# Performance work log

Measured on AMD Instinct MI355X. Metric: run time of the kernel, lower is better.

The kernel has to match this reference:

```python
import jax, jax.numpy as jnp
import numpy as np

NUM_CLASSES = 81
POS_THR = 0.5
NEG_THR = 0.1
TOTAL = 512        # roi_training_total_num_samples
MAX_POS = 128      # roi_training_max_pos_samples
SIGMA = 1.0
CLS_W = 1.0
REG_W = 1.0
BBOX_MEAN = jnp.array([0.0, 0.0, 0.0, 0.0], dtype=jnp.float32)
BBOX_STD = jnp.array([0.1, 0.1, 0.2, 0.2], dtype=jnp.float32)
N_PROP = 65536
N_GT = 64
IMG = 1024.0


def _make_boxes(key, n):
    k1, k2, k3, k4 = jax.random.split(key, 4)
    cx = jax.random.uniform(k1, (n,), minval=150.0, maxval=870.0)
    cy = jax.random.uniform(k2, (n,), minval=150.0, maxval=870.0)
    w = jax.random.uniform(k3, (n,), minval=40.0, maxval=200.0)
    h = jax.random.uniform(k4, (n,), minval=40.0, maxval=200.0)
    return jnp.stack([cx - w / 2, cy - h / 2, cx + w / 2, cy + h / 2], axis=1)


def _sanitize(b):
    b = jnp.clip(b, 0.0, IMG)
    x1, y1, x2, y2 = b[:, 0], b[:, 1], b[:, 2], b[:, 3]
    return jnp.stack([x1, y1, jnp.maximum(x2, x1 + 1.0), jnp.maximum(y2, y1 + 1.0)], axis=1)


def setup_inputs() -> dict:
    key = jax.random.key(0)
    ks = jax.random.split(key, 8)
    gt_bboxes = _make_boxes(ks[0], N_GT)
    gt_labels = jax.random.randint(ks[1], (N_GT,), 1, NUM_CLASSES).astype(jnp.int32)
    # proposals: 4096 light-jittered gt copies (positives), 16384 medium jitter
    # (iou in [0.1,0.5) band), rest random -> realistic pos/neg mix
    n_pos, n_med = 4096, 16384
    base_pos = gt_bboxes[jnp.arange(n_pos) % N_GT]
    base_med = gt_bboxes[jnp.arange(n_med) % N_GT]
    p_pos = base_pos + jax.random.uniform(ks[2], (n_pos, 4), minval=-15.0, maxval=15.0)
    p_med = base_med + jax.random.uniform(ks[3], (n_med, 4), minval=-80.0, maxval=80.0)
    p_rand = _make_boxes(ks[4], N_PROP - n_pos - n_med)
    rpn_proposals_bboxes = _sanitize(jnp.concatenate([p_pos, p_med, p_rand], axis=0))
    roi_score = jax.random.normal(ks[5], (N_PROP, NUM_CLASSES), dtype=jnp.float32)
    roi_bboxes_txtytwth = jax.random.normal(ks[6], (N_PROP, NUM_CLASSES, 4), dtype=jnp.float32)
    image_shape = jnp.array([IMG, IMG], dtype=jnp.float32)
    return {
        "image_shape": image_shape,
        "rpn_proposals_bboxes": rpn_proposals_bboxes,
        "roi_score": roi_score,
        "roi_bboxes_txtytwth": roi_bboxes_txtytwth,
        "gt_bboxes": gt_bboxes,
        "gt_labels": gt_labels,
    }


def pairwise_iou(a, b):
    # a: [N,4], b: [G,4] in (x1,y1,x2,y2)
    area_a = (a[:, 2] - a[:, 0]) * (a[:, 3] - a[:, 1])
    area_b = (b[:, 2] - b[:, 0]) * (b[:, 3] - b[:, 1])
    lt = jnp.maximum(a[:, None, :2], b[None, :, :2])
    rb = jnp.minimum(a[:, None, 2:], b[None, :, 2:])
    wh = jnp.clip(rb - lt, 0.0)
    inter = wh[..., 0] * wh[..., 1]
    return inter / (area_a[:, None] + area_b[None, :] - inter + 1e-8)


def encode_bbox(props, gts):
    pw = props[:, 2] - props[:, 0]
    ph = props[:, 3] - props[:, 1]
    pcx = props[:, 0] + 0.5 * pw
    pcy = props[:, 1] + 0.5 * ph
    gw = gts[:, 2] - gts[:, 0]
    gh = gts[:, 3] - gts[:, 1]
    gcx = gts[:, 0] + 0.5 * gw
    gcy = gts[:, 1] + 0.5 * gh
    t = jnp.stack([(gcx - pcx) / pw, (gcy - pcy) / ph,
                   jnp.log(gw / pw), jnp.log(gh / ph)], axis=1)
    return (t - BBOX_MEAN) / BBOX_STD


def smooth_l1(diff, sigma):
    s2 = sigma * sigma
    ad = jnp.abs(diff)
    return jnp.where(ad < 1.0 / s2, 0.5 * s2 * diff * diff, ad - 0.5 / s2)


def sample_rois(proposals, gt_bboxes):
    # IoU-threshold sampler with deterministic (index-order) selection and
    # static output size TOTAL. Returns (idx[TOTAL], labels[TOTAL], gt_idx[TOTAL], num_pos)
    n = proposals.shape[0]
    iou = pairwise_iou(proposals, gt_bboxes)          # [N,G]
    max_iou = iou.max(axis=1)
    gt_idx = jnp.argmax(iou, axis=1)
    pos_mask = max_iou >= POS_THR
    neg_mask = (max_iou < POS_THR) & (max_iou >= NEG_THR)
    num_pos = jnp.minimum(pos_mask.sum(), MAX_POS)
    ar = jnp.arange(n)
    pos_order = jnp.argsort(jnp.where(pos_mask, ar, ar + n))
    neg_order = jnp.argsort(jnp.where(neg_mask, ar, ar + n))
    slot = jnp.arange(TOTAL)
    is_pos = slot < num_pos
    idx = jnp.where(is_pos, pos_order[jnp.clip(slot, 0, n - 1)],
                    neg_order[jnp.clip(slot - num_pos, 0, n - 1)])
    labels = is_pos.astype(jnp.int32)
    return idx, labels, gt_idx[idx], is_pos


def reference(image_shape, rpn_proposals_bboxes, roi_score, roi_bboxes_txtytwth,
              gt_bboxes, gt_labels):
    idx, labels, gt_sel, is_pos = sample_rois(rpn_proposals_bboxes, gt_bboxes)
    # classification loss over all TOTAL samples (negatives get label 0)
    logits = roi_score[idx]                              # [T,C]
    cls_labels = gt_labels[gt_sel] * labels              # [T]
    logp = jax.nn.log_softmax(logits, axis=-1)
    ce = -jnp.take_along_axis(logp, cls_labels[:, None], axis=1)[:, 0]
    cls_loss = CLS_W * ce.mean()
    pred = roi_bboxes_txtytwth[idx, gt_sel]              # [T,4]
    targets = encode_bbox(jax.lax.stop_gradient(rpn_proposals_bboxes[idx]),
                          jax.lax.stop_gradient(gt_bboxes[gt_sel]))
    sl1 = smooth_l1(pred - targets, SIGMA)               # [T,4]
    m = is_pos.astype(pred.dtype)[:, None]
    reg_loss = REG_W * jnp.sum(sl1 * m) / float(TOTAL)
    return (cls_loss, reg_loss)
```

## Files before the change

kernel.cpp:

```cpp
#include <hip/hip_runtime.h>
#include <cstdint>

#define N_PROP 65536
#define N_GT 64
#define NUM_CLASSES 81
#define TOTAL_SLOTS 512
#define MAX_POS 128

__global__ __launch_bounds__(256) void iou_cat_kernel(
    const float* __restrict__ props,
    const float* __restrict__ gts,
    int* __restrict__ code_ws) {
  __shared__ float4 sgt[N_GT];
  __shared__ float sarea[N_GT];
  int tid = threadIdx.x;
  if (tid < N_GT) {
    float4 g = ((const float4*)gts)[tid];
    sgt[tid] = g;
    sarea[tid] = (g.z - g.x) * (g.w - g.y);
  }
  __syncthreads();
  int i = blockIdx.x * blockDim.x + tid;
  if (i >= N_PROP) return;
  float4 p = ((const float4*)props)[i];
  float area_a = (p.z - p.x) * (p.w - p.y);
  float best = -1.0f;
  int bg = 0;
  for (int g = 0; g < N_GT; ++g) {
    float4 q = sgt[g];
    float ltx = fmaxf(p.x, q.x);
    float lty = fmaxf(p.y, q.y);
    float rbx = fminf(p.z, q.z);
    float rby = fminf(p.w, q.w);
    float wx = fmaxf(rbx - ltx, 0.0f);
    float wy = fmaxf(rby - lty, 0.0f);
    float inter = wx * wy;
    float denom = area_a + sarea[g] - inter + 1e-8f;
    float iou = inter / denom;
    if (iou > best) { best = iou; bg = g; }
  }
  int cat = (best >= 0.5f) ? 2 : ((best >= 0.1f) ? 1 : 0);
  code_ws[i] = (cat << 8) | bg;
}

__global__ __launch_bounds__(1024) void select_loss_kernel(
    const float* __restrict__ props,
    const float* __restrict__ scores,
    const float* __restrict__ deltas,
    const float* __restrict__ gts,
    const int* __restrict__ gt_labels,
    const int* __restrict__ code_ws,
    float* __restrict__ out) {
  __shared__ int pos_list[MAX_POS];
  __shared__ int neg_list[TOTAL_SLOTS];
  __shared__ int nn_list[TOTAL_SLOTS];
  __shared__ int wsum_p[16], wsum_n[16], wsum_nn[16];
  __shared__ int base_p, base_n, base_nn;
  __shared__ float red[1024];
  __shared__ float ce_sum_sh;

  int tid = threadIdx.x;
  if (tid == 0) { base_p = 0; base_n = 0; base_nn = 0; }
  __syncthreads();

  int lane = tid & 63;
  int wave = tid >> 6;
  uint64_t lmask = (1ULL << lane) - 1ULL;

  for (int c = 0; c < N_PROP / 1024; ++c) {
    if (base_p >= MAX_POS && base_n >= TOTAL_SLOTS && base_nn >= TOTAL_SLOTS)
      break;
    int i = c * 1024 + tid;
    int code = code_ws[i];
    int cat = code >> 8;
    bool isp = (cat == 2);
    bool isn = (cat == 1);
    bool isnn = !isn;
    uint64_t bp = __ballot(isp);
    uint64_t bn = __ballot(isn);
    uint64_t bnn = __ballot(isnn);
    if (lane == 0) {
      wsum_p[wave] = __popcll(bp);
      wsum_n[wave] = __popcll(bn);
      wsum_nn[wave] = __popcll(bnn);
    }
    __syncthreads();
    int wp = 0, wn = 0, wnn = 0;
    for (int w = 0; w < wave; ++w) {
      wp += wsum_p[w];
      wn += wsum_n[w];
      wnn += wsum_nn[w];
    }
    if (isp) {
      int r = base_p + wp + __popcll(bp & lmask);
      if (r < MAX_POS) pos_list[r] = i;
    }
    if (isn) {
      int r = base_n + wn + __popcll(bn & lmask);
      if (r < TOTAL_SLOTS) neg_list[r] = i;
    }
    if (isnn) {
      int r = base_nn + wnn + __popcll(bnn & lmask);
      if (r < TOTAL_SLOTS) nn_list[r] = i;
    }
    __syncthreads();
    if (tid == 0) {
      int tp = 0, tn = 0, tnn = 0;
      for (int w = 0; w < 16; ++w) {
        tp += wsum_p[w];
        tn += wsum_n[w];
        tnn += wsum_nn[w];
      }
      base_p += tp;
      base_n += tn;
      base_nn += tnn;
    }
    __syncthreads();
  }

  int num_pos = min(base_p, MAX_POS);
  int neg_total = base_n;

  float ce = 0.0f, reg = 0.0f;
  if (tid < TOTAL_SLOTS) {
    int s = tid;
    bool is_pos = (s < num_pos);
    int i;
    if (is_pos) {
      i = pos_list[s];
    } else {
      int j = s - num_pos;
      i = (j < neg_total) ? neg_list[j] : nn_list[j - neg_total];
    }
    int g = code_ws[i] & 0xFF;

    int cls = is_pos ? gt_labels[g] : 0;
    const float* row = scores + (size_t)i * NUM_CLASSES;
    float m = -INFINITY;
    for (int k = 0; k < NUM_CLASSES; ++k) m = fmaxf(m, row[k]);
    float sum = 0.0f;
    for (int k = 0; k < NUM_CLASSES; ++k) sum += expf(row[k] - m);
    ce = -(row[cls] - m - logf(sum));

    const float* pr = props + 4 * i;
    float pw = pr[2] - pr[0];
    float ph = pr[3] - pr[1];
    float pcx = pr[0] + 0.5f * pw;
    float pcy = pr[1] + 0.5f * ph;
    const float* gb = gts + 4 * g;
    float gw = gb[2] - gb[0];
    float gh = gb[3] - gb[1];
    float gcx = gb[0] + 0.5f * gw;
    float gcy = gb[1] + 0.5f * gh;
    float t0 = ((gcx - pcx) / pw) / 0.1f;
    float t1 = ((gcy - pcy) / ph) / 0.1f;
    float t2 = logf(gw / pw) / 0.2f;
    float t3 = logf(gh / ph) / 0.2f;
    const float* dd = deltas + ((size_t)i * NUM_CLASSES + (size_t)g) * 4;
    float d0 = dd[0] - t0;
    float d1 = dd[1] - t1;
    float d2 = dd[2] - t2;
    float d3 = dd[3] - t3;
    float sl = 0.0f;
    float a;
    a = fabsf(d0); sl += (a < 1.0f) ? 0.5f * d0 * d0 : a - 0.5f;
    a = fabsf(d1); sl += (a < 1.0f) ? 0.5f * d1 * d1 : a - 0.5f;
    a = fabsf(d2); sl += (a < 1.0f) ? 0.5f * d2 * d2 : a - 0.5f;
    a = fabsf(d3); sl += (a < 1.0f) ? 0.5f * d3 * d3 : a - 0.5f;
    if (is_pos) reg = sl;
  }

  red[tid] = ce;
  __syncthreads();
  for (int off = 512; off >= 1; off >>= 1) {
    if (tid < off) red[tid] += red[tid + off];
    __syncthreads();
  }
  if (tid == 0) ce_sum_sh = red[0];
  __syncthreads();

  red[tid] = reg;
  __syncthreads();
  for (int off = 512; off >= 1; off >>= 1) {
    if (tid < off) red[tid] += red[tid + off];
    __syncthreads();
  }
  if (tid == 0) {
    out[0] = ce_sum_sh / (float)TOTAL_SLOTS;
    out[1] = red[0] / (float)TOTAL_SLOTS;
  }
}

extern "C" void kernel_launch(void* const* d_in, const int* in_sizes, int n_in,
                              void* d_out, int out_size, void* d_ws, size_t ws_size,
                              hipStream_t stream) {
  (void)in_sizes; (void)n_in; (void)out_size; (void)ws_size;
  const float* props = (const float*)d_in[1];
  const float* scores = (const float*)d_in[2];
  const float* deltas = (const float*)d_in[3];
  const float* gts = (const float*)d_in[4];
  const int* gt_labels = (const int*)d_in[5];
  float* out = (float*)d_out;
  int* code_ws = (int*)d_ws;

  iou_cat_kernel<<<N_PROP / 256, 256, 0, stream>>>(props, gts, code_ws);
  select_loss_kernel<<<1, 1024, 0, stream>>>(props, scores, deltas, gts,
                                             gt_labels, code_ws, out);
}
```

Before: 182.5 us.

## Split selection and loss into separate kernels with per-sample wavefront loss

Moves the per-sample cross-entropy and regression loss out of the single-block selection kernel into a new kernel with one 64-thread block per selected sample. Each block loads its score row in parallel, reduces max and sum-exp with wave shuffles, and accumulates both losses into the output with atomics. The selection kernel writes packed indices to workspace and zeroes the output. This removes the serial 81-element loops and the long block reductions on one workgroup, at the cost of an extra launch, atomic ordering nondeterminism, and __expf approximation.

```diff
diff --git a/kernel.cpp b/kernel.cpp
--- a/kernel.cpp
+++ b/kernel.cpp
@@ -21,7 +21,6 @@
   }
   __syncthreads();
   int i = blockIdx.x * blockDim.x + tid;
-  if (i >= N_PROP) return;
   float4 p = ((const float4*)props)[i];
   float area_a = (p.z - p.x) * (p.w - p.y);
   float best = -1.0f;
@@ -43,21 +42,15 @@
   code_ws[i] = (cat << 8) | bg;
 }
 
-__global__ __launch_bounds__(1024) void select_loss_kernel(
-    const float* __restrict__ props,
-    const float* __restrict__ scores,
-    const float* __restrict__ deltas,
-    const float* __restrict__ gts,
-    const int* __restrict__ gt_labels,
+__global__ __launch_bounds__(1024) void select_kernel(
     const int* __restrict__ code_ws,
+    int* __restrict__ sel_ws,
     float* __restrict__ out) {
   __shared__ int pos_list[MAX_POS];
   __shared__ int neg_list[TOTAL_SLOTS];
   __shared__ int nn_list[TOTAL_SLOTS];
   __shared__ int wsum_p[16], wsum_n[16], wsum_nn[16];
   __shared__ int base_p, base_n, base_nn;
-  __shared__ float red[1024];
-  __shared__ float ce_sum_sh;
 
   int tid = threadIdx.x;
   if (tid == 0) { base_p = 0; base_n = 0; base_nn = 0; }
@@ -121,7 +114,6 @@
   int num_pos = min(base_p, MAX_POS);
   int neg_total = base_n;
 
-  float ce = 0.0f, reg = 0.0f;
   if (tid < TOTAL_SLOTS) {
     int s = tid;
     bool is_pos = (s < num_pos);
@@ -133,61 +125,74 @@
       i = (j < neg_total) ? neg_list[j] : nn_list[j - neg_total];
     }
     int g = code_ws[i] & 0xFF;
-
+    sel_ws[s] = i | (g << 17) | ((is_pos ? 1 : 0) << 23);
+  }
+  if (tid < 2) out[tid] = 0.0f;
+}
+
+__global__ __launch_bounds__(64) void loss_kernel(
+    const float* __restrict__ props,
+    const float* __restrict__ scores,
+    const float* __restrict__ deltas,
+    const float* __restrict__ gts,
+    const int* __restrict__ gt_labels,
+    const int* __restrict__ sel_ws,
+    float* __restrict__ out) {
+  int s = blockIdx.x;
+  int packed = sel_ws[s];
+  int i = packed & 0x1FFFF;
+  int g = (packed >> 17) & 0x3F;
+  bool is_pos = (packed >> 23) & 1;
+
+  int lane = threadIdx.x;
+  const float* row = scores + (size_t)i * NUM_CLASSES;
+  float v1 = row[lane];
+  bool has2 = (lane + 64) < NUM_CLASSES;
+  float v2 = has2 ? row[lane + 64] : -INFINITY;
+
+  float m = fmaxf(v1, v2);
+  #pragma unroll
+  for (int off = 32; off >= 1; off >>= 1)
+    m = fmaxf(m, __shfl_xor(m, off));
+
+  float e = __expf(v1 - m) + (has2 ? __expf(v2 - m) : 0.0f);
+  #pragma unroll
+  for (int off = 32; off >= 1; off >>= 1)
+    e += __shfl_xor(e, off);
+
+  if (lane == 0) {
     int cls = is_pos ? gt_labels[g] : 0;
-    const float* row = scores + (size_t)i * NUM_CLASSES;
-    float m = -INFINITY;
-    for (int k = 0; k < NUM_CLASSES; ++k) m = fmaxf(m, row[k]);
-    float sum = 0.0f;
-    for (int k = 0; k < NUM_CLASSES; ++k) sum += expf(row[k] - m);
-    ce = -(row[cls] - m - logf(sum));
-
-    const float* pr = props + 4 * i;
-    float pw = pr[2] - pr[0];
-    float ph = pr[3] - pr[1];
-    float pcx = pr[0] + 0.5f * pw;
-    float pcy = pr[1] + 0.5f * ph;
-    const float* gb = gts + 4 * g;
-    float gw = gb[2] - gb[0];
-    float gh = gb[3] - gb[1];
-    float gcx = gb[0] + 0.5f * gw;
-    float gcy = gb[1] + 0.5f * gh;
-    float t0 = ((gcx - pcx) / pw) / 0.1f;
-    float t1 = ((gcy - pcy) / ph) / 0.1f;
-    float t2 = logf(gw / pw) / 0.2f;
-    float t3 = logf(gh / ph) / 0.2f;
-    const float* dd = deltas + ((size_t)i * NUM_CLASSES + (size_t)g) * 4;
-    float d0 = dd[0] - t0;
-    float d1 = dd[1] - t1;
-    float d2 = dd[2] - t2;
-    float d3 = dd[3] - t3;
-    float sl = 0.0f;
-    float a;
-    a = fabsf(d0); sl += (a < 1.0f) ? 0.5f * d0 * d0 : a - 0.5f;
-    a = fabsf(d1); sl += (a < 1.0f) ? 0.5f * d1 * d1 : a - 0.5f;
-    a = fabsf(d2); sl += (a < 1.0f) ? 0.5f * d2 * d2 : a - 0.5f;
-    a = fabsf(d3); sl += (a < 1.0f) ? 0.5f * d3 * d3 : a - 0.5f;
-    if (is_pos) reg = sl;
-  }
-
-  red[tid] = ce;
-  __syncthreads();
-  for (int off = 512; off >= 1; off >>= 1) {
-    if (tid < off) red[tid] += red[tid + off];
-    __syncthreads();
-  }
-  if (tid == 0) ce_sum_sh = red[0];
-  __syncthreads();
-
-  red[tid] = reg;
-  __syncthreads();
-  for (int off = 512; off >= 1; off >>= 1) {
-    if (tid < off) red[tid] += red[tid + off];
-    __syncthreads();
-  }
-  if (tid == 0) {
-    out[0] = ce_sum_sh / (float)TOTAL_SLOTS;
-    out[1] = red[0] / (float)TOTAL_SLOTS;
+    float ce = -(row[cls] - m - logf(e));
+    atomicAdd(out + 0, ce * (1.0f / (float)TOTAL_SLOTS));
+
+    if (is_pos) {
+      const float* pr = props + 4 * i;
+      float pw = pr[2] - pr[0];
+      float ph = pr[3] - pr[1];
+      float pcx = pr[0] + 0.5f * pw;
+      float pcy = pr[1] + 0.5f * ph;
+      const float* gb = gts + 4 * g;
+      float gw = gb[2] - gb[0];
+      float gh = gb[3] - gb[1];
+      float gcx = gb[0] + 0.5f * gw;
+      float gcy = gb[1] + 0.5f * gh;
+      float t0 = ((gcx - pcx) / pw) / 0.1f;
+      float t1 = ((gcy - pcy) / ph) / 0.1f;
+      float t2 = logf(gw / pw) / 0.2f;
+      float t3 = logf(gh / ph) / 0.2f;
+      const float* dd = deltas + ((size_t)i * NUM_CLASSES + (size_t)g) * 4;
+      float d0 = dd[0] - t0;
+      float d1 = dd[1] - t1;
+      float d2 = dd[2] - t2;
+      float d3 = dd[3] - t3;
+      float sl = 0.0f;
+      float a;
+      a = fabsf(d0); sl += (a < 1.0f) ? 0.5f * d0 * d0 : a - 0.5f;
+      a = fabsf(d1); sl += (a < 1.0f) ? 0.5f * d1 * d1 : a - 0.5f;
+      a = fabsf(d2); sl += (a < 1.0f) ? 0.5f * d2 * d2 : a - 0.5f;
+      a = fabsf(d3); sl += (a < 1.0f) ? 0.5f * d3 * d3 : a - 0.5f;
+      atomicAdd(out + 1, sl * (1.0f / (float)TOTAL_SLOTS));
+    }
   }
 }
 
@@ -202,8 +207,10 @@
   const int* gt_labels = (const int*)d_in[5];
   float* out = (float*)d_out;
   int* code_ws = (int*)d_ws;
+  int* sel_ws = code_ws + N_PROP;
 
   iou_cat_kernel<<<N_PROP / 256, 256, 0, stream>>>(props, gts, code_ws);
-  select_loss_kernel<<<1, 1024, 0, stream>>>(props, scores, deltas, gts,
-                                             gt_labels, code_ws, out);
-}
+  select_kernel<<<1, 1024, 0, stream>>>(code_ws, sel_ws, out);
+  loss_kernel<<<TOTAL_SLOTS, 64, 0, stream>>>(props, scores, deltas, gts,
+                                              gt_labels, sel_ws, out);
+}
```

After: 149.6 us. 1.22x faster.
